# Optimization experiments

Measured on AMD Instinct MI355X. Metric: run time of the kernel, lower is better.

The kernel has to match this reference:

```python
import jax, jax.numpy as jnp
import numpy as np

KH, KW = 3, 3
STRIDE, PAD, DIL = 1, 1, 1


def setup_inputs() -> dict:
    key = jax.random.key(0)
    k1, k2, k3 = jax.random.split(key, 3)
    B, C, H, W, O = 8, 128, 64, 64, 128
    x = jax.random.normal(k1, (B, C, H, W), jnp.float32)
    # offset layout: [B, 2*K, Ho, Wo], pairs (dy, dx) per kernel tap
    offset = jax.random.normal(k2, (B, 2 * KH * KW, H, W), jnp.float32)
    n = C * KH * KW
    stdv = 1.0 / np.sqrt(n)
    weight = jax.random.uniform(k3, (O, C, KH, KW), jnp.float32, -stdv, stdv)
    bias = jnp.zeros((O,), jnp.float32)
    return {"x": x, "offset": offset, "weight": weight, "bias": bias}


def _deform_conv(x, offset, weight, bias):
    B, C, H, W = x.shape
    O = weight.shape[0]
    K = KH * KW
    Ho = (H + 2 * PAD - DIL * (KH - 1) - 1) // STRIDE + 1
    Wo = (W + 2 * PAD - DIL * (KW - 1) - 1) // STRIDE + 1

    off = offset.reshape(B, K, 2, Ho, Wo)  # (dy, dx) per tap

    # base sampling grid for each kernel tap: [K, Ho, Wo]
    hs = jnp.arange(Ho, dtype=jnp.float32) * STRIDE - PAD
    ws = jnp.arange(Wo, dtype=jnp.float32) * STRIDE - PAD
    ki = jnp.arange(KH, dtype=jnp.float32) * DIL
    kj = jnp.arange(KW, dtype=jnp.float32) * DIL
    base_y = (ki[:, None, None, None] + hs[None, None, :, None])  # [KH,1,Ho,1]
    base_x = (kj[None, :, None, None] + ws[None, None, None, :])  # [1,KW,1,Wo]
    base_y = jnp.broadcast_to(base_y, (KH, KW, Ho, Wo)).reshape(K, Ho, Wo)
    base_x = jnp.broadcast_to(base_x, (KH, KW, Ho, Wo)).reshape(K, Ho, Wo)

    py = base_y[None] + off[:, :, 0]  # [B,K,Ho,Wo]
    px = base_x[None] + off[:, :, 1]

    y0 = jnp.floor(py)
    x0 = jnp.floor(px)
    ly = py - y0  # fractional parts
    lx = px - x0
    y0i = y0.astype(jnp.int32)
    x0i = x0.astype(jnp.int32)

    flat = x.reshape(B, C, H * W)

    def gather(yi, xi, w):
        # zero outside the image (DCN zero-padding semantics)
        valid = (yi >= 0) & (yi < H) & (xi >= 0) & (xi < W)
        idx = jnp.clip(yi, 0, H - 1) * W + jnp.clip(xi, 0, W - 1)  # [B,K,Ho,Wo]
        g = jnp.take_along_axis(flat, idx.reshape(B, 1, -1), axis=2)
        g = g.reshape(B, C, K, Ho, Wo)
        wmask = (w * valid.astype(x.dtype))[:, None]  # [B,1,K,Ho,Wo]
        return g * wmask

    # bilinear accumulation over 4 corners -> im2col columns [B,C,K,Ho,Wo]
    cols = gather(y0i, x0i, (1 - ly) * (1 - lx))
    cols = cols + gather(y0i, x0i + 1, (1 - ly) * lx)
    cols = cols + gather(y0i + 1, x0i, ly * (1 - lx))
    cols = cols + gather(y0i + 1, x0i + 1, ly * lx)

    out = jnp.einsum('ock,bckhw->bohw', weight.reshape(O, C, K), cols)
    return out + bias[None, :, None, None]


def reference(x, offset, weight, bias):
    return _deform_conv(x, offset, weight, bias)
```

## Files before the change

### kernel.cpp

```cpp
#include <hip/hip_runtime.h>


#define BB 8
#define CC 128
#define HH 64
#define WW 64
#define OO 128
#define KTAPS 9
#define WLDS_STRIDE 136

typedef __attribute__((ext_vector_type(8))) short bf16x8;
typedef __attribute__((ext_vector_type(4))) float f32x4;

__device__ __forceinline__ unsigned short f2bf(float f) {
    unsigned u = __float_as_uint(f);
    u += 0x7FFFu + ((u >> 16) & 1u);
    return (unsigned short)(u >> 16);
}
__device__ __forceinline__ float bf2f(unsigned u16) {
    return __uint_as_float(u16 << 16);
}

__global__ __launch_bounds__(256)
void transpose_x_kernel(const float* __restrict__ x, unsigned short* __restrict__ xt) {
    __shared__ float tile[WW * 129];
    const int b = blockIdx.x >> 6;
    const int h = blockIdx.x & 63;
    const float* src = x + ((size_t)b * CC * HH + h) * WW;
    for (int i = threadIdx.x; i < CC * WW; i += 256) {
        const int c = i >> 6;
        const int w = i & 63;
        tile[w * 129 + c] = src[(size_t)c * (HH * WW) + w];
    }
    __syncthreads();
    unsigned short* dst = xt + ((size_t)b * HH + h) * WW * CC;
    for (int i = threadIdx.x; i < (CC / 2) * WW; i += 256) {
        const int w  = i >> 6;
        const int cp = i & 63;
        const float f0 = tile[w * 129 + 2 * cp];
        const float f1 = tile[w * 129 + 2 * cp + 1];
        const unsigned pack = (unsigned)f2bf(f0) | ((unsigned)f2bf(f1) << 16);
        *reinterpret_cast<unsigned*>(&dst[(size_t)w * CC + 2 * cp]) = pack;
    }
}

__global__ __launch_bounds__(256)
void transpose_w_kernel(const float* __restrict__ wgt, unsigned short* __restrict__ wt) {
    const int idx = blockIdx.x * 256 + threadIdx.x;
    if (idx >= OO * CC * KTAPS) return;
    const int o   = idx / (CC * KTAPS);
    const int r   = idx - o * (CC * KTAPS);
    const int c   = r / KTAPS;
    const int tap = r - c * KTAPS;
    wt[((size_t)o * KTAPS + tap) * CC + c] = f2bf(wgt[idx]);
}

__global__ __launch_bounds__(256, 2)
void dcn_mfma_kernel(const unsigned short* __restrict__ xt,
                     const unsigned short* __restrict__ wt,
                     const float* __restrict__ offset,
                     const float* __restrict__ bias,
                     float* __restrict__ out) {
    __shared__ __align__(16) int4   sA[KTAPS * WW];
    __shared__ __align__(16) float4 sWt[KTAPS * WW];
    __shared__ __align__(16) unsigned short wlds[OO * WLDS_STRIDE];

    const int t  = threadIdx.x;
    const int b  = blockIdx.x >> 6;
    const int ho = blockIdx.x & 63;

    for (int s = t; s < KTAPS * WW; s += 256) {
        const int k  = s >> 6;
        const int wo = s & 63;
        const int ki = k / 3;
        const int kj = k - ki * 3;
        const float dy = offset[(((size_t)b * 18 + 2 * k    ) * 64 + ho) * 64 + wo];
        const float dx = offset[(((size_t)b * 18 + 2 * k + 1) * 64 + ho) * 64 + wo];
        const float py = (float)(ho - 1 + ki) + dy;
        const float px = (float)(wo - 1 + kj) + dx;
        const float y0f = floorf(py);
        const float x0f = floorf(px);
        const float ly = py - y0f;
        const float lx = px - x0f;
        const int y0 = (int)y0f, x0 = (int)x0f;
        const int y1 = y0 + 1,   x1 = x0 + 1;
        const bool vy0 = (y0 >= 0) && (y0 < HH);
        const bool vy1 = (y1 >= 0) && (y1 < HH);
        const bool vx0 = (x0 >= 0) && (x0 < WW);
        const bool vx1 = (x1 >= 0) && (x1 < WW);
        const int cy0 = min(max(y0, 0), HH - 1);
        const int cy1 = min(max(y1, 0), HH - 1);
        const int cx0 = min(max(x0, 0), WW - 1);
        const int cx1 = min(max(x1, 0), WW - 1);
        float4 w4;
        w4.x = (vy0 && vx0) ? (1.f - ly) * (1.f - lx) : 0.f;
        w4.y = (vy0 && vx1) ? (1.f - ly) * lx         : 0.f;
        w4.z = (vy1 && vx0) ? ly * (1.f - lx)         : 0.f;
        w4.w = (vy1 && vx1) ? ly * lx                 : 0.f;
        sWt[s] = w4;
        sA[s] = make_int4(((cy0 * WW + cx0) * CC) * 2, ((cy0 * WW + cx1) * CC) * 2,
                          ((cy1 * WW + cx0) * CC) * 2, ((cy1 * WW + cx1) * CC) * 2);
    }

    f32x4 acc[8];
#pragma unroll
    for (int nt = 0; nt < 8; ++nt) acc[nt] = (f32x4){0.f, 0.f, 0.f, 0.f};

    const int lane = t & 63;
    const int wave = t >> 6;
    const int lm   = lane & 15;
    const int quad = lane >> 4;
    const char* xb = (const char*)(xt + (size_t)b * HH * WW * CC);

    __syncthreads();

    for (int tap = 0; tap < KTAPS; ++tap) {
        {
            const int seg  = t & 15;
            const int orow = t >> 4;
#pragma unroll
            for (int i = 0; i < 8; ++i) {
                const int o = orow + i * 16;
                const uint4 v = *reinterpret_cast<const uint4*>(
                    wt + ((size_t)o * KTAPS + tap) * CC + seg * 8);
                *reinterpret_cast<uint4*>(&wlds[o * WLDS_STRIDE + seg * 8]) = v;
            }
        }
        __syncthreads();

        const int rec = (tap << 6) + (wave << 4) + lm;
        const int4   a4 = sA[rec];
        const float4 w4 = sWt[rec];

#pragma unroll
        for (int c0 = 0; c0 < CC; c0 += 32) {
            const int cb = (c0 + quad * 8) * 2;
            const uint4 v00 = *reinterpret_cast<const uint4*>(xb + a4.x + cb);
            const uint4 v01 = *reinterpret_cast<const uint4*>(xb + a4.y + cb);
            const uint4 v10 = *reinterpret_cast<const uint4*>(xb + a4.z + cb);
            const uint4 v11 = *reinterpret_cast<const uint4*>(xb + a4.w + cb);
            const unsigned* u00 = reinterpret_cast<const unsigned*>(&v00);
            const unsigned* u01 = reinterpret_cast<const unsigned*>(&v01);
            const unsigned* u10 = reinterpret_cast<const unsigned*>(&v10);
            const unsigned* u11 = reinterpret_cast<const unsigned*>(&v11);
            unsigned afu[4];
#pragma unroll
            for (int j = 0; j < 4; ++j) {
                const unsigned p00 = u00[j], p01 = u01[j], p10 = u10[j], p11 = u11[j];
                const float lo = w4.x * bf2f(p00 & 0xFFFFu) + w4.y * bf2f(p01 & 0xFFFFu)
                               + w4.z * bf2f(p10 & 0xFFFFu) + w4.w * bf2f(p11 & 0xFFFFu);
                const float hi = w4.x * bf2f(p00 >> 16) + w4.y * bf2f(p01 >> 16)
                               + w4.z * bf2f(p10 >> 16) + w4.w * bf2f(p11 >> 16);
                afu[j] = (unsigned)f2bf(lo) | ((unsigned)f2bf(hi) << 16);
            }
            const bf16x8 afrag = *reinterpret_cast<const bf16x8*>(afu);
#pragma unroll
            for (int nt = 0; nt < 8; ++nt) {
                const bf16x8 bfrag = *reinterpret_cast<const bf16x8*>(
                    &wlds[(nt * 16 + lm) * WLDS_STRIDE + c0 + quad * 8]);
                acc[nt] = __builtin_amdgcn_mfma_f32_16x16x32_bf16(afrag, bfrag, acc[nt], 0, 0, 0);
            }
        }
        __syncthreads();
    }

    const int wo = (wave << 4) + quad * 4;
#pragma unroll
    for (int nt = 0; nt < 8; ++nt) {
        const int o = (nt << 4) + lm;
        const float bv = bias[o];
        float* op = out + ((((size_t)b * OO + o) * HH + ho) << 6) + wo;
        float4 v = {acc[nt][0] + bv, acc[nt][1] + bv, acc[nt][2] + bv, acc[nt][3] + bv};
        *reinterpret_cast<float4*>(op) = v;
    }
}

extern "C" void kernel_launch(void* const* d_in, const int* in_sizes, int n_in,
                              void* d_out, int out_size, void* d_ws, size_t ws_size,
                              hipStream_t stream) {
    const float* x      = (const float*)d_in[0];
    const float* offset = (const float*)d_in[1];
    const float* wgt    = (const float*)d_in[2];
    const float* bias   = (const float*)d_in[3];
    float* out = (float*)d_out;

    unsigned short* xt = (unsigned short*)d_ws;
    unsigned short* wt = xt + (size_t)BB * HH * WW * CC;

    hipLaunchKernelGGL(transpose_w_kernel, dim3((OO * CC * KTAPS + 255) / 256), dim3(256),
                       0, stream, wgt, wt);
    hipLaunchKernelGGL(transpose_x_kernel, dim3(BB * HH), dim3(256), 0, stream, x, xt);
    hipLaunchKernelGGL(dcn_mfma_kernel, dim3(BB * HH), dim3(256), 0, stream,
                       xt, wt, offset, bias, out);
}
```

Before: 134.3 us.

## Split DCN rows across two blocks, vectorize transposes, stage output through LDS

The main kernel now launches two blocks per output row. Each block covers 32 output columns, and its four waves split as 2 M-tiles by 2 halves of the output channels, with launch bounds raised to 4 blocks per CU for more parallelism and occupancy. Per-tap sampling data is stored compactly as fractional parts and short coordinates, and the bilinear weights and addresses are recomputed in registers. Results go through an LDS scratch buffer so each lane writes contiguous float4 runs per output channel. The x and weight transpose kernels are vectorized with float4/uint4 accesses. The trade-off is that each block now reloads the full weight tile per tap for half the pixels, which doubles weight traffic into LDS.

```diff
diff --git a/kernel.cpp b/kernel.cpp
--- a/kernel.cpp
+++ b/kernel.cpp
@@ -23,91 +23,105 @@
 
 __global__ __launch_bounds__(256)
 void transpose_x_kernel(const float* __restrict__ x, unsigned short* __restrict__ xt) {
-    __shared__ float tile[WW * 129];
+    __shared__ float tile[WW * 132];
+    const int t = threadIdx.x;
     const int b = blockIdx.x >> 6;
     const int h = blockIdx.x & 63;
     const float* src = x + ((size_t)b * CC * HH + h) * WW;
-    for (int i = threadIdx.x; i < CC * WW; i += 256) {
-        const int c = i >> 6;
-        const int w = i & 63;
-        tile[w * 129 + c] = src[(size_t)c * (HH * WW) + w];
+    {
+        const int wq = t & 15;
+        const int cb = t >> 4;
+#pragma unroll
+        for (int it = 0; it < 8; ++it) {
+            const int c = it * 16 + cb;
+            const float4 v = *reinterpret_cast<const float4*>(src + (size_t)c * (HH * WW) + wq * 4);
+            tile[(wq * 4 + 0) * 132 + c] = v.x;
+            tile[(wq * 4 + 1) * 132 + c] = v.y;
+            tile[(wq * 4 + 2) * 132 + c] = v.z;
+            tile[(wq * 4 + 3) * 132 + c] = v.w;
+        }
     }
     __syncthreads();
     unsigned short* dst = xt + ((size_t)b * HH + h) * WW * CC;
-    for (int i = threadIdx.x; i < (CC / 2) * WW; i += 256) {
-        const int w  = i >> 6;
-        const int cp = i & 63;
-        const float f0 = tile[w * 129 + 2 * cp];
-        const float f1 = tile[w * 129 + 2 * cp + 1];
-        const unsigned pack = (unsigned)f2bf(f0) | ((unsigned)f2bf(f1) << 16);
-        *reinterpret_cast<unsigned*>(&dst[(size_t)w * CC + 2 * cp]) = pack;
+    {
+        const int cg = t & 15;
+        const int wb = t >> 4;
+#pragma unroll
+        for (int it = 0; it < 4; ++it) {
+            const int w = it * 16 + wb;
+            const float2 f0 = *reinterpret_cast<const float2*>(&tile[w * 132 + cg * 8 + 0]);
+            const float2 f1 = *reinterpret_cast<const float2*>(&tile[w * 132 + cg * 8 + 2]);
+            const float2 f2 = *reinterpret_cast<const float2*>(&tile[w * 132 + cg * 8 + 4]);
+            const float2 f3 = *reinterpret_cast<const float2*>(&tile[w * 132 + cg * 8 + 6]);
+            uint4 p;
+            p.x = (unsigned)f2bf(f0.x) | ((unsigned)f2bf(f0.y) << 16);
+            p.y = (unsigned)f2bf(f1.x) | ((unsigned)f2bf(f1.y) << 16);
+            p.z = (unsigned)f2bf(f2.x) | ((unsigned)f2bf(f2.y) << 16);
+            p.w = (unsigned)f2bf(f3.x) | ((unsigned)f2bf(f3.y) << 16);
+            *reinterpret_cast<uint4*>(&dst[(size_t)w * CC + cg * 8]) = p;
+        }
     }
 }
 
 __global__ __launch_bounds__(256)
 void transpose_w_kernel(const float* __restrict__ wgt, unsigned short* __restrict__ wt) {
-    const int idx = blockIdx.x * 256 + threadIdx.x;
-    if (idx >= OO * CC * KTAPS) return;
-    const int o   = idx / (CC * KTAPS);
-    const int r   = idx - o * (CC * KTAPS);
-    const int c   = r / KTAPS;
-    const int tap = r - c * KTAPS;
-    wt[((size_t)o * KTAPS + tap) * CC + c] = f2bf(wgt[idx]);
-}
-
-__global__ __launch_bounds__(256, 2)
+    const int id = blockIdx.x * 256 + threadIdx.x;
+    if (id >= OO * KTAPS * 16) return;
+    const int cg  = id & 15;
+    const int r   = id >> 4;
+    const int tap = r % KTAPS;
+    const int o   = r / KTAPS;
+    const float* s = wgt + ((size_t)o * CC + cg * 8) * KTAPS + tap;
+    unsigned u[4];
+#pragma unroll
+    for (int j = 0; j < 4; ++j) {
+        const unsigned short lo = f2bf(s[(2 * j)     * KTAPS]);
+        const unsigned short hi = f2bf(s[(2 * j + 1) * KTAPS]);
+        u[j] = (unsigned)lo | ((unsigned)hi << 16);
+    }
+    *reinterpret_cast<uint4*>(&wt[((size_t)o * KTAPS + tap) * CC + cg * 8]) =
+        make_uint4(u[0], u[1], u[2], u[3]);
+}
+
+__global__ __launch_bounds__(256, 4)
 void dcn_mfma_kernel(const unsigned short* __restrict__ xt,
                      const unsigned short* __restrict__ wt,
                      const float* __restrict__ offset,
                      const float* __restrict__ bias,
                      float* __restrict__ out) {
-    __shared__ __align__(16) int4   sA[KTAPS * WW];
-    __shared__ __align__(16) float4 sWt[KTAPS * WW];
     __shared__ __align__(16) unsigned short wlds[OO * WLDS_STRIDE];
+    __shared__ __align__(8)  float2 sLL[KTAPS * 32];
+    __shared__ __align__(4)  short2 sYX[KTAPS * 32];
 
     const int t  = threadIdx.x;
-    const int b  = blockIdx.x >> 6;
-    const int ho = blockIdx.x & 63;
-
-    for (int s = t; s < KTAPS * WW; s += 256) {
-        const int k  = s >> 6;
-        const int wo = s & 63;
-        const int ki = k / 3;
-        const int kj = k - ki * 3;
+    const int b  = blockIdx.x >> 7;
+    const int ho = (blockIdx.x >> 1) & 63;
+    const int mh = blockIdx.x & 1;
+
+    for (int s = t; s < KTAPS * 32; s += 256) {
+        const int k   = s >> 5;
+        const int wol = s & 31;
+        const int wo  = mh * 32 + wol;
+        const int ki  = k / 3;
+        const int kj  = k - ki * 3;
         const float dy = offset[(((size_t)b * 18 + 2 * k    ) * 64 + ho) * 64 + wo];
         const float dx = offset[(((size_t)b * 18 + 2 * k + 1) * 64 + ho) * 64 + wo];
         const float py = (float)(ho - 1 + ki) + dy;
         const float px = (float)(wo - 1 + kj) + dx;
         const float y0f = floorf(py);
         const float x0f = floorf(px);
-        const float ly = py - y0f;
-        const float lx = px - x0f;
-        const int y0 = (int)y0f, x0 = (int)x0f;
-        const int y1 = y0 + 1,   x1 = x0 + 1;
-        const bool vy0 = (y0 >= 0) && (y0 < HH);
-        const bool vy1 = (y1 >= 0) && (y1 < HH);
-        const bool vx0 = (x0 >= 0) && (x0 < WW);
-        const bool vx1 = (x1 >= 0) && (x1 < WW);
-        const int cy0 = min(max(y0, 0), HH - 1);
-        const int cy1 = min(max(y1, 0), HH - 1);
-        const int cx0 = min(max(x0, 0), WW - 1);
-        const int cx1 = min(max(x1, 0), WW - 1);
-        float4 w4;
-        w4.x = (vy0 && vx0) ? (1.f - ly) * (1.f - lx) : 0.f;
-        w4.y = (vy0 && vx1) ? (1.f - ly) * lx         : 0.f;
-        w4.z = (vy1 && vx0) ? ly * (1.f - lx)         : 0.f;
-        w4.w = (vy1 && vx1) ? ly * lx                 : 0.f;
-        sWt[s] = w4;
-        sA[s] = make_int4(((cy0 * WW + cx0) * CC) * 2, ((cy0 * WW + cx1) * CC) * 2,
-                          ((cy1 * WW + cx0) * CC) * 2, ((cy1 * WW + cx1) * CC) * 2);
-    }
-
-    f32x4 acc[8];
-#pragma unroll
-    for (int nt = 0; nt < 8; ++nt) acc[nt] = (f32x4){0.f, 0.f, 0.f, 0.f};
+        sLL[s] = make_float2(py - y0f, px - x0f);
+        sYX[s] = make_short2((short)(int)y0f, (short)(int)x0f);
+    }
+
+    f32x4 acc[4];
+#pragma unroll
+    for (int nt = 0; nt < 4; ++nt) acc[nt] = (f32x4){0.f, 0.f, 0.f, 0.f};
 
     const int lane = t & 63;
     const int wave = t >> 6;
+    const int mi   = wave & 1;
+    const int nh   = wave >> 1;
     const int lm   = lane & 15;
     const int quad = lane >> 4;
     const char* xb = (const char*)(xt + (size_t)b * HH * WW * CC);
@@ -126,19 +140,39 @@
                 *reinterpret_cast<uint4*>(&wlds[o * WLDS_STRIDE + seg * 8]) = v;
             }
         }
+
+        const int rec = (tap << 5) + (mi << 4) + lm;
+        const float2 ll = sLL[rec];
+        const short2 yx = sYX[rec];
+        const int y0 = yx.x, x0 = yx.y;
+        const int y1 = y0 + 1, x1 = x0 + 1;
+        const float ly = ll.x, lx = ll.y;
+        const bool vy0 = ((unsigned)y0 < (unsigned)HH);
+        const bool vy1 = ((unsigned)y1 < (unsigned)HH);
+        const bool vx0 = ((unsigned)x0 < (unsigned)WW);
+        const bool vx1 = ((unsigned)x1 < (unsigned)WW);
+        const float w00 = (vy0 && vx0) ? (1.f - ly) * (1.f - lx) : 0.f;
+        const float w01 = (vy0 && vx1) ? (1.f - ly) * lx         : 0.f;
+        const float w10 = (vy1 && vx0) ? ly * (1.f - lx)         : 0.f;
+        const float w11 = (vy1 && vx1) ? ly * lx                 : 0.f;
+        const int cy0 = min(max(y0, 0), HH - 1);
+        const int cy1 = min(max(y1, 0), HH - 1);
+        const int cx0 = min(max(x0, 0), WW - 1);
+        const int cx1 = min(max(x1, 0), WW - 1);
+        const int o00 = ((cy0 << 6) + cx0) << 8;
+        const int o01 = ((cy0 << 6) + cx1) << 8;
+        const int o10 = ((cy1 << 6) + cx0) << 8;
+        const int o11 = ((cy1 << 6) + cx1) << 8;
+
         __syncthreads();
-
-        const int rec = (tap << 6) + (wave << 4) + lm;
-        const int4   a4 = sA[rec];
-        const float4 w4 = sWt[rec];
 
 #pragma unroll
         for (int c0 = 0; c0 < CC; c0 += 32) {
             const int cb = (c0 + quad * 8) * 2;
-            const uint4 v00 = *reinterpret_cast<const uint4*>(xb + a4.x + cb);
-            const uint4 v01 = *reinterpret_cast<const uint4*>(xb + a4.y + cb);
-            const uint4 v10 = *reinterpret_cast<const uint4*>(xb + a4.z + cb);
-            const uint4 v11 = *reinterpret_cast<const uint4*>(xb + a4.w + cb);
+            const uint4 v00 = *reinterpret_cast<const uint4*>(xb + o00 + cb);
+            const uint4 v01 = *reinterpret_cast<const uint4*>(xb + o01 + cb);
+            const uint4 v10 = *reinterpret_cast<const uint4*>(xb + o10 + cb);
+            const uint4 v11 = *reinterpret_cast<const uint4*>(xb + o11 + cb);
             const unsigned* u00 = reinterpret_cast<const unsigned*>(&v00);
             const unsigned* u01 = reinterpret_cast<const unsigned*>(&v01);
             const unsigned* u10 = reinterpret_cast<const unsigned*>(&v10);
@@ -147,31 +181,43 @@
 #pragma unroll
             for (int j = 0; j < 4; ++j) {
                 const unsigned p00 = u00[j], p01 = u01[j], p10 = u10[j], p11 = u11[j];
-                const float lo = w4.x * bf2f(p00 & 0xFFFFu) + w4.y * bf2f(p01 & 0xFFFFu)
-                               + w4.z * bf2f(p10 & 0xFFFFu) + w4.w * bf2f(p11 & 0xFFFFu);
-                const float hi = w4.x * bf2f(p00 >> 16) + w4.y * bf2f(p01 >> 16)
-                               + w4.z * bf2f(p10 >> 16) + w4.w * bf2f(p11 >> 16);
+                const float lo = w00 * bf2f(p00 & 0xFFFFu) + w01 * bf2f(p01 & 0xFFFFu)
+                               + w10 * bf2f(p10 & 0xFFFFu) + w11 * bf2f(p11 & 0xFFFFu);
+                const float hi = w00 * bf2f(p00 >> 16) + w01 * bf2f(p01 >> 16)
+                               + w10 * bf2f(p10 >> 16) + w11 * bf2f(p11 >> 16);
                 afu[j] = (unsigned)f2bf(lo) | ((unsigned)f2bf(hi) << 16);
             }
             const bf16x8 afrag = *reinterpret_cast<const bf16x8*>(afu);
 #pragma unroll
-            for (int nt = 0; nt < 8; ++nt) {
+            for (int nt = 0; nt < 4; ++nt) {
                 const bf16x8 bfrag = *reinterpret_cast<const bf16x8*>(
-                    &wlds[(nt * 16 + lm) * WLDS_STRIDE + c0 + quad * 8]);
+                    &wlds[(nh * 64 + nt * 16 + lm) * WLDS_STRIDE + c0 + quad * 8]);
                 acc[nt] = __builtin_amdgcn_mfma_f32_16x16x32_bf16(afrag, bfrag, acc[nt], 0, 0, 0);
             }
         }
         __syncthreads();
     }
 
-    const int wo = (wave << 4) + quad * 4;
-#pragma unroll
-    for (int nt = 0; nt < 8; ++nt) {
-        const int o = (nt << 4) + lm;
+    float* scr = reinterpret_cast<float*>(wlds) + wave * (64 * 20);
+#pragma unroll
+    for (int nt = 0; nt < 4; ++nt) {
+        const int o_l = nt * 16 + lm;
+        f32x4 v = acc[nt];
+        *reinterpret_cast<float4*>(&scr[o_l * 20 + quad * 4]) =
+            make_float4(v[0], v[1], v[2], v[3]);
+    }
+    __syncthreads();
+    {
+        const int o = nh * 64 + lane;
         const float bv = bias[o];
-        float* op = out + ((((size_t)b * OO + o) * HH + ho) << 6) + wo;
-        float4 v = {acc[nt][0] + bv, acc[nt][1] + bv, acc[nt][2] + bv, acc[nt][3] + bv};
-        *reinterpret_cast<float4*>(op) = v;
+        float* op = out + (((size_t)(b * OO + o) * HH + ho) << 6) + mh * 32 + mi * 16;
+        const float* sr = reinterpret_cast<const float*>(wlds) + wave * (64 * 20) + lane * 20;
+#pragma unroll
+        for (int j = 0; j < 4; ++j) {
+            const float4 f = *reinterpret_cast<const float4*>(sr + j * 4);
+            *reinterpret_cast<float4*>(op + j * 4) =
+                make_float4(f.x + bv, f.y + bv, f.z + bv, f.w + bv);
+        }
     }
 }
 
@@ -187,9 +233,9 @@
     unsigned short* xt = (unsigned short*)d_ws;
     unsigned short* wt = xt + (size_t)BB * HH * WW * CC;
 
-    hipLaunchKernelGGL(transpose_w_kernel, dim3((OO * CC * KTAPS + 255) / 256), dim3(256),
+    hipLaunchKernelGGL(transpose_w_kernel, dim3((OO * KTAPS * 16 + 255) / 256), dim3(256),
                        0, stream, wgt, wt);
     hipLaunchKernelGGL(transpose_x_kernel, dim3(BB * HH), dim3(256), 0, stream, x, xt);
-    hipLaunchKernelGGL(dcn_mfma_kernel, dim3(BB * HH), dim3(256), 0, stream,
+    hipLaunchKernelGGL(dcn_mfma_kernel, dim3(BB * HH * 2), dim3(256), 0, stream,
                        xt, wt, offset, bias, out);
 }
```

New measurement: 160.7 us. 1.2x slower.
